# Kernel optimization log

Hardware: AMD Instinct MI355X
Metric: run time of the kernel (lower is better)

The kernel has to match this reference:

```python
import jax, jax.numpy as jnp
import numpy as np

BS, QLEN, DIM, NH = 2, 2048, 1024, 16
HD = DIM // NH


def setup_inputs() -> dict:
    key = jax.random.key(0)
    ks = jax.random.split(key, 6)
    std = 0.02
    return {
        "x": jax.random.normal(ks[0], (BS, QLEN, DIM), dtype=jnp.float32),
        "mask": jnp.ones((BS, QLEN), dtype=jnp.float32),
        "Wq": jax.random.normal(ks[1], (DIM, DIM), dtype=jnp.float32) * std,
        "bq": jnp.zeros((DIM,), dtype=jnp.float32),
        "Wk": jax.random.normal(ks[2], (DIM, DIM), dtype=jnp.float32) * std,
        "bk": jnp.zeros((DIM,), dtype=jnp.float32),
        "Wv": jax.random.normal(ks[3], (DIM, DIM), dtype=jnp.float32) * std,
        "bv": jnp.zeros((DIM,), dtype=jnp.float32),
        "Wo": jax.random.normal(ks[4], (DIM, DIM), dtype=jnp.float32) * std,
        "bo": jnp.zeros((DIM,), dtype=jnp.float32),
    }


def reference(x, mask, Wq, bq, Wk, bk, Wv, bv, Wo, bo):
    bs, qlen, dim = x.shape
    # project and split heads: [bs, nh, len, hd]
    def split_heads(t):
        return t.reshape(bs, -1, NH, HD).transpose(0, 2, 1, 3)

    q = split_heads(x @ Wq + bq) / jnp.sqrt(jnp.float32(HD))
    k = split_heads(x @ Wk + bk)
    v = split_heads(x @ Wv + bv)

    scores = jnp.einsum("bhqd,bhkd->bhqk", q, k)  # [bs, nh, qlen, klen]
    m = mask.reshape(bs, 1, 1, -1)  # 2D mask -> broadcast over heads and q
    scores = scores - 1e30 * (1.0 - m)
    weights = jax.nn.softmax(scores, axis=-1)
    # dropout p=0.0 at inference -> no-op; head_mask is None
    context = jnp.einsum("bhqk,bhkd->bhqd", weights, v)
    context = context.transpose(0, 2, 1, 3).reshape(bs, qlen, NH * HD)
    return context @ Wo + bo
```

## Files before the change

### kernel.cpp

```cpp
#include <hip/hip_runtime.h>
#include <stdint.h>

#define BSZ  2
#define SEQ  2048
#define DIM  1024
#define NHD  16
#define HD   64
#define MTOT (BSZ*SEQ)

using short8  = __attribute__((ext_vector_type(8))) short;
using floatx4 = __attribute__((ext_vector_type(4))) float;

#define QSCALE 0.18033688011112042f
#define BIGM   1.44e30f

__device__ __forceinline__ unsigned short f2bf(float f) {
    unsigned int u = __float_as_uint(f);
    u += 0x7fffu + ((u >> 16) & 1u);
    return (unsigned short)(u >> 16);
}
__device__ __forceinline__ unsigned int pk2r(float a, float b) {
    unsigned int ua = __float_as_uint(a) + 0x8000u;
    unsigned int ub = __float_as_uint(b) + 0x8000u;
    return __builtin_amdgcn_perm(ub, ua, 0x07060302);
}
__device__ __forceinline__ unsigned int cvtpk(float a, float b) {
    unsigned int r;
    asm("v_cvt_pk_bf16_f32 %0, %1, %2" : "=v"(r) : "v"(a), "v"(b));
    return r;
}

__device__ __forceinline__ void gll16(const void* g, const void* lds) {
    unsigned int loff = (unsigned int)(unsigned long long)lds;
    __builtin_amdgcn_global_load_lds(
        (const __attribute__((address_space(1))) unsigned int*)g,
        (__attribute__((address_space(3))) unsigned int*)loff, 16, 0, 0);
}

__global__ __launch_bounds__(256)
void conv_x(const float* __restrict__ X, const float* __restrict__ mask,
            unsigned short* __restrict__ Xbf, float* __restrict__ Pen) {
    size_t i = ((size_t)blockIdx.x * 256 + threadIdx.x) * 8;
    float4 a = *(const float4*)(X + i);
    float4 b = *(const float4*)(X + i + 4);
    uint4 u = {pk2r(a.x, a.y), pk2r(a.z, a.w), pk2r(b.x, b.y), pk2r(b.z, b.w)};
    *(uint4*)(Xbf + i) = u;
    if (blockIdx.x < 2) {
        const size_t j = ((size_t)blockIdx.x * 256 + threadIdx.x) * 8;
        float4 m0 = *(const float4*)(mask + j);
        float4 m1 = *(const float4*)(mask + j + 4);
        float4 r0 = {__builtin_fmaf(m0.x, BIGM, -BIGM), __builtin_fmaf(m0.y, BIGM, -BIGM),
                     __builtin_fmaf(m0.z, BIGM, -BIGM), __builtin_fmaf(m0.w, BIGM, -BIGM)};
        float4 r1 = {__builtin_fmaf(m1.x, BIGM, -BIGM), __builtin_fmaf(m1.y, BIGM, -BIGM),
                     __builtin_fmaf(m1.z, BIGM, -BIGM), __builtin_fmaf(m1.w, BIGM, -BIGM)};
        *(float4*)(Pen + j)     = r0;
        *(float4*)(Pen + j + 4) = r1;
    }
}

__global__ __launch_bounds__(256)
void conv_wt(const float* __restrict__ Wq, const float* __restrict__ Wk,
             const float* __restrict__ Wv, const float* __restrict__ Wo,
             unsigned short* __restrict__ Wt3, unsigned short* __restrict__ Wto)
{
    __shared__ float tile[64 * 65];
    const int z = blockIdx.z;
    const float* W = (z == 0) ? Wq : (z == 1) ? Wk : (z == 2) ? Wv : Wo;
    unsigned short* out = (z < 3) ? (Wt3 + (size_t)z * DIM * DIM) : Wto;
    const int k0 = blockIdx.x * 64, n0 = blockIdx.y * 64;
    const int t = threadIdx.x;
    const int r = t >> 2, c0 = (t & 3) * 16;
#pragma unroll
    for (int j = 0; j < 4; ++j) {
        float4 v = *(const float4*)&W[(size_t)(k0 + r) * DIM + n0 + c0 + j * 4];
        tile[r * 65 + c0 + j * 4 + 0] = v.x;
        tile[r * 65 + c0 + j * 4 + 1] = v.y;
        tile[r * 65 + c0 + j * 4 + 2] = v.z;
        tile[r * 65 + c0 + j * 4 + 3] = v.w;
    }
    __syncthreads();
    unsigned int p[8];
#pragma unroll
    for (int j = 0; j < 8; ++j)
        p[j] = pk2r(tile[(c0 + 2 * j) * 65 + r], tile[(c0 + 2 * j + 1) * 65 + r]);
    uint4 u0 = {p[0], p[1], p[2], p[3]}, u1 = {p[4], p[5], p[6], p[7]};
    unsigned short* dst = out + (size_t)(n0 + r) * DIM + k0 + c0;
    *(uint4*)dst = u0;
    *(uint4*)(dst + 8) = u1;
}

__global__ __launch_bounds__(256)
void qkv_gemm(const unsigned short* __restrict__ Xbf,
              const unsigned short* __restrict__ Wt3,
              const float* __restrict__ bq, const float* __restrict__ bk,
              const float* __restrict__ bv,
              unsigned short* __restrict__ Qb,
              unsigned short* __restrict__ Kb,
              unsigned short* __restrict__ VbT)
{
    __shared__ unsigned short As[2][128 * 32];
    __shared__ unsigned short Bs[2][128 * 32];

    const int t = threadIdx.x, w = t >> 6, lane = t & 63;
    const int lm = lane & 15, grp = lane >> 4;
    const int wm = w >> 1, wn = w & 1;
    const int m0 = blockIdx.x * 128;
    const int mat = blockIdx.y >> 3;
    const int n0 = (blockIdx.y & 7) * 128;
    const unsigned short* Bg = Wt3 + (size_t)mat * DIM * DIM;
    const int lr = lane >> 2, lc = (lane & 3) * 8;
    const int r0 = w * 16;
    const bool swap = (mat != 2);

    const unsigned short* xs0 = Xbf + (size_t)(m0 + r0 + lr) * DIM + lc;
    const unsigned short* xs1 = Xbf + (size_t)(m0 + 64 + r0 + lr) * DIM + lc;
    const unsigned short* ws0 = Bg  + (size_t)(n0 + r0 + lr) * DIM + lc;
    const unsigned short* ws1 = Bg  + (size_t)(n0 + 64 + r0 + lr) * DIM + lc;

    const unsigned short* afb[2];
    const unsigned short* bfb[2];
#pragma unroll
    for (int u = 0; u < 2; ++u) {
        afb[u] = &As[u][(wm * 64 + lm) * 32 + grp * 8];
        bfb[u] = &Bs[u][(wn * 64 + lm) * 32 + grp * 8];
    }

    floatx4 acc[4][4];
#pragma unroll
    for (int i = 0; i < 4; ++i)
#pragma unroll
        for (int j = 0; j < 4; ++j) acc[i][j] = (floatx4){0.f, 0.f, 0.f, 0.f};

#define QKV_STAGE(BUF) do {                                    \
        gll16(xs0, &As[BUF][r0 * 32]);                         \
        gll16(xs1, &As[BUF][(64 + r0) * 32]);                  \
        gll16(ws0, &Bs[BUF][r0 * 32]);                         \
        gll16(ws1, &Bs[BUF][(64 + r0) * 32]);                  \
        xs0 += 32; xs1 += 32; ws0 += 32; ws1 += 32;            \
    } while (0)

#define QKV_BODY(CUR) do {                                                    \
        __syncthreads();                                                      \
        QKV_STAGE(CUR ^ 1);                                                   \
        short8 af[4], bf[4];                                                  \
        _Pragma("unroll")                                                     \
        for (int mt = 0; mt < 4; ++mt)                                        \
            af[mt] = *(const short8*)(afb[CUR] + mt * 512);                   \
        _Pragma("unroll")                                                     \
        for (int nt = 0; nt < 4; ++nt)                                        \
            bf[nt] = *(const short8*)(bfb[CUR] + nt * 512);                   \
        if (swap) {                                                           \
            _Pragma("unroll")                                                 \
            for (int mt = 0; mt < 4; ++mt)                                    \
                _Pragma("unroll")                                             \
                for (int nt = 0; nt < 4; ++nt)                                \
                    acc[mt][nt] = __builtin_amdgcn_mfma_f32_16x16x32_bf16(    \
                        bf[nt], af[mt], acc[mt][nt], 0, 0, 0);                \
        } else {                                                              \
            _Pragma("unroll")                                                 \
            for (int mt = 0; mt < 4; ++mt)                                    \
                _Pragma("unroll")                                             \
                for (int nt = 0; nt < 4; ++nt)                                \
                    acc[mt][nt] = __builtin_amdgcn_mfma_f32_16x16x32_bf16(    \
                        af[mt], bf[nt], acc[mt][nt], 0, 0, 0);                \
        }                                                                     \
    } while (0)

    QKV_STAGE(0);
#pragma unroll 1
    for (int it = 0; it < DIM / 64; ++it) {
        QKV_BODY(0);
        QKV_BODY(1);
    }
#undef QKV_BODY
#undef QKV_STAGE

    if (mat == 2) {
#pragma unroll
        for (int nt = 0; nt < 4; ++nt) {
            const int c = n0 + wn * 64 + nt * 16 + lm;
            const float bb = bv[c];
            const int h = c >> 6, d = c & 63;
#pragma unroll
            for (int mt = 0; mt < 4; ++mt) {
                const int r = m0 + wm * 64 + mt * 16 + grp * 4;
                const int b = r >> 11, s = r & 2047;
                const int si = s & 63, sb = s & ~63;
                const int cg = si >> 4, g = (si >> 2) & 3;
                const int unit = (((cg & 1) << 2) | g) ^ (d & 7);
                const int sph = sb + unit * 8 + ((cg >> 1) << 2);
                uint2 pv;
                pv.x = pk2r(acc[mt][nt][0] + bb, acc[mt][nt][1] + bb);
                pv.y = pk2r(acc[mt][nt][2] + bb, acc[mt][nt][3] + bb);
                *(uint2*)&VbT[(((size_t)(b * NHD + h)) * HD + d) * SEQ + sph] = pv;
            }
        }
    } else {
        const float* bias = (mat == 0) ? bq : bk;
        unsigned short* dst = (mat == 0) ? Qb : Kb;
        const float sc = (mat == 0) ? QSCALE : 1.0f;
#pragma unroll
        for (int nt = 0; nt < 4; ++nt) {
            const int c0 = n0 + wn * 64 + nt * 16 + grp * 4;
            float4 bb = *(const float4*)&bias[c0];
            const int h = c0 >> 6, d0 = c0 & 63;
#pragma unroll
            for (int mt = 0; mt < 4; ++mt) {
                const int r = m0 + wm * 64 + mt * 16 + lm;
                const int b = r >> 11, s = r & 2047;
                uint2 pv;
                pv.x = pk2r((acc[mt][nt][0] + bb.x) * sc, (acc[mt][nt][1] + bb.y) * sc);
                pv.y = pk2r((acc[mt][nt][2] + bb.z) * sc, (acc[mt][nt][3] + bb.w) * sc);
                const int dd = (mat == 0) ? d0
                             : ((((d0 >> 3) ^ (s & 7)) << 3) | (d0 & 7));
                *(uint2*)&dst[(((size_t)(b * NHD + h)) * SEQ + s) * HD + dd] = pv;
            }
        }
    }
}

__global__ __launch_bounds__(256, 4)
void attn(const unsigned short* __restrict__ Qb,
          const unsigned short* __restrict__ Kb,
          const unsigned short* __restrict__ VbT,
          const float* __restrict__ Pen,
          unsigned short* __restrict__ Cb)
{
    __shared__ unsigned short Kt[2][64 * 64];
    __shared__ unsigned short Vt[2][64 * 64];

    const int t = threadIdx.x, w = t >> 6, lane = t & 63;
    const int lm = lane & 15, grp = lane >> 4;
    const int x7 = lm & 7;

    const int lin = blockIdx.y * (int)gridDim.x + blockIdx.x;
    const int swz = (lin & 7) * ((SEQ / 64) * (BSZ * NHD) / 8) + (lin >> 3);
    const int bh = swz >> 5, b = bh >> 4, h = bh & 15;
    const int q0 = (swz & 31) * 64;

    short8 qf[2];
    {
        const unsigned short* qrow = Qb + ((size_t)bh * SEQ + q0 + w * 16 + lm) * HD;
        qf[0] = *(const short8*)(qrow + grp * 8);
        qf[1] = *(const short8*)(qrow + 32 + grp * 8);
    }

    const unsigned int one2 = 0x3f803f80u;
    uint4 onesu = {one2, one2, one2, one2};
    short8 ones = *(const short8*)&onesu;

    floatx4 oacc[4];
#pragma unroll
    for (int i = 0; i < 4; ++i) oacc[i] = (floatx4){0.f, 0.f, 0.f, 0.f};
    floatx4 lacc = (floatx4){0.f, 0.f, 0.f, 0.f};

    const unsigned short* Kg = Kb + (size_t)bh * SEQ * HD;
    const unsigned short* Vg = VbT + (size_t)bh * HD * SEQ;
    const int srow = lane >> 3, scol = (lane & 7) * 8;

    const unsigned short* kp0 = Kg + (size_t)(w * 16 + srow) * HD + scol;
    const unsigned short* kp1 = kp0 + 8 * HD;
    const unsigned short* vp0 = Vg + (size_t)(w * 16 + srow) * SEQ + scol;
    const unsigned short* vp1 = vp0 + 8 * SEQ;

    gll16(kp0, &Kt[0][(w * 16) * 64]);
    gll16(kp1, &Kt[0][(w * 16 + 8) * 64]);
    gll16(vp0, &Vt[0][(w * 16) * 64]);
    gll16(vp1, &Vt[0][(w * 16 + 8) * 64]);
    kp0 += 64 * HD; kp1 += 64 * HD; vp0 += 64; vp1 += 64;

    const unsigned short* kba[2]; const unsigned short* kbb[2];
    const unsigned short* vba[2]; const unsigned short* vbb[2];
#pragma unroll
    for (int u = 0; u < 2; ++u) {
        kba[u] = &Kt[u][lm * 64 + ((grp    ) ^ x7) * 8];
        kbb[u] = &Kt[u][lm * 64 + ((4 + grp) ^ x7) * 8];
        vba[u] = &Vt[u][lm * 64 + ((grp    ) ^ x7) * 8];
        vbb[u] = &Vt[u][lm * 64 + ((4 + grp) ^ x7) * 8];
    }
    const float* mp = Pen + (size_t)b * SEQ + grp * 4;

#define ATTN_BODY(CUR) do {                                                   \
        __syncthreads();                                                      \
        gll16(kp0, &Kt[CUR ^ 1][(w * 16) * 64]);                              \
        gll16(kp1, &Kt[CUR ^ 1][(w * 16 + 8) * 64]);                          \
        gll16(vp0, &Vt[CUR ^ 1][(w * 16) * 64]);                              \
        gll16(vp1, &Vt[CUR ^ 1][(w * 16 + 8) * 64]);                          \
        kp0 += 64 * HD; kp1 += 64 * HD; vp0 += 64; vp1 += 64;                 \
        float4 mdv[4];                                                        \
        _Pragma("unroll")                                                     \
        for (int cg = 0; cg < 4; ++cg)                                        \
            mdv[cg] = *(const float4*)(mp + cg * 16);                         \
        mp += 64;                                                             \
        floatx4 sv[4];                                                        \
        __builtin_amdgcn_s_setprio(1);                                        \
        _Pragma("unroll")                                                     \
        for (int cg = 0; cg < 4; ++cg) {                                      \
            short8 a0 = *(const short8*)(kba[CUR] + cg * 1024);               \
            short8 a1 = *(const short8*)(kbb[CUR] + cg * 1024);               \
            floatx4 s = (floatx4){mdv[cg].x, mdv[cg].y, mdv[cg].z, mdv[cg].w}; \
            s = __builtin_amdgcn_mfma_f32_16x16x32_bf16(a0, qf[0], s, 0, 0, 0); \
            s = __builtin_amdgcn_mfma_f32_16x16x32_bf16(a1, qf[1], s, 0, 0, 0); \
            sv[cg] = s;                                                       \
        }                                                                     \
        __builtin_amdgcn_s_setprio(0);                                        \
        short8 vf[4][2];                                                      \
        _Pragma("unroll")                                                     \
        for (int dg = 0; dg < 4; ++dg) {                                      \
            vf[dg][0] = *(const short8*)(vba[CUR] + dg * 1024);               \
            vf[dg][1] = *(const short8*)(vbb[CUR] + dg * 1024);               \
        }                                                                     \
        float p[4][4];                                                        \
        _Pragma("unroll")                                                     \
        for (int cg = 0; cg < 4; ++cg) {                                      \
            p[cg][0] = __builtin_exp2f(sv[cg][0]);                            \
            p[cg][1] = __builtin_exp2f(sv[cg][1]);                            \
            p[cg][2] = __builtin_exp2f(sv[cg][2]);                            \
            p[cg][3] = __builtin_exp2f(sv[cg][3]);                            \
        }                                                                     \
        uint4 u0, u1;                                                         \
        u0.x = cvtpk(p[0][0], p[0][1]); u0.y = cvtpk(p[0][2], p[0][3]);       \
        u0.z = cvtpk(p[2][0], p[2][1]); u0.w = cvtpk(p[2][2], p[2][3]);       \
        u1.x = cvtpk(p[1][0], p[1][1]); u1.y = cvtpk(p[1][2], p[1][3]);       \
        u1.z = cvtpk(p[3][0], p[3][1]); u1.w = cvtpk(p[3][2], p[3][3]);       \
        short8 ap0 = *(const short8*)&u0;                                     \
        short8 ap1 = *(const short8*)&u1;                                     \
        __builtin_amdgcn_s_setprio(1);                                        \
        _Pragma("unroll")                                                     \
        for (int dg = 0; dg < 4; ++dg) {                                      \
            oacc[dg] = __builtin_amdgcn_mfma_f32_16x16x32_bf16(ap0, vf[dg][0], oacc[dg], 0, 0, 0); \
            oacc[dg] = __builtin_amdgcn_mfma_f32_16x16x32_bf16(ap1, vf[dg][1], oacc[dg], 0, 0, 0); \
        }                                                                     \
        lacc = __builtin_amdgcn_mfma_f32_16x16x32_bf16(ap0, ones, lacc, 0, 0, 0); \
        lacc = __builtin_amdgcn_mfma_f32_16x16x32_bf16(ap1, ones, lacc, 0, 0, 0); \
        __builtin_amdgcn_s_setprio(0);                                        \
    } while (0)

#pragma unroll 1
    for (int it = 0; it < SEQ / 128; ++it) {
        ATTN_BODY(0);
        ATTN_BODY(1);
    }
#undef ATTN_BODY

    float inv[4];
#pragma unroll
    for (int r = 0; r < 4; ++r) inv[r] = (lacc[r] > 0.f) ? 1.0f / lacc[r] : 0.f;
#pragma unroll
    for (int dg = 0; dg < 4; ++dg)
#pragma unroll
        for (int r = 0; r < 4; ++r) {
            const int s = q0 + w * 16 + grp * 4 + r;
            Cb[((size_t)(b * SEQ + s)) * DIM + h * HD + dg * 16 + lm] =
                f2bf(oacc[dg][r] * inv[r]);
        }
}

__global__ __launch_bounds__(256)
void out_gemm(const unsigned short* __restrict__ Cb,
              const unsigned short* __restrict__ Wto,
              const float* __restrict__ bo,
              float* __restrict__ out)
{
    __shared__ unsigned short As[2][128 * 32];
    __shared__ unsigned short Bs[2][64 * 32];

    const int t = threadIdx.x, w = t >> 6, lane = t & 63;
    const int lm = lane & 15, grp = lane >> 4;
    const int m0 = blockIdx.x * 128;
    const int n0 = blockIdx.y * 64;
    const int lr = lane >> 2, lc = (lane & 3) * 8;
    const int r0 = w * 16;

    const unsigned short* cs0 = Cb  + (size_t)(m0 + r0 + lr) * DIM + lc;
    const unsigned short* cs1 = Cb  + (size_t)(m0 + 64 + r0 + lr) * DIM + lc;
    const unsigned short* ws0 = Wto + (size_t)(n0 + r0 + lr) * DIM + lc;

    const unsigned short* afb[2];
    const unsigned short* bfb[2];
#pragma unroll
    for (int u = 0; u < 2; ++u) {
        afb[u] = &As[u][(w * 32 + lm) * 32 + grp * 8];
        bfb[u] = &Bs[u][lm * 32 + grp * 8];
    }

    floatx4 acc[2][4];
#pragma unroll
    for (int i = 0; i < 2; ++i)
#pragma unroll
        for (int j = 0; j < 4; ++j) acc[i][j] = (floatx4){0.f, 0.f, 0.f, 0.f};

#define OUT_STAGE(BUF) do {                                    \
        gll16(cs0, &As[BUF][r0 * 32]);                         \
        gll16(cs1, &As[BUF][(64 + r0) * 32]);                  \
        gll16(ws0, &Bs[BUF][r0 * 32]);                         \
        cs0 += 32; cs1 += 32; ws0 += 32;                       \
    } while (0)

#define OUT_BODY(CUR) do {                                                    \
        __syncthreads();                                                      \
        OUT_STAGE(CUR ^ 1);                                                   \
        short8 af[2], bf[4];                                                  \
        _Pragma("unroll")                                                     \
        for (int mt = 0; mt < 2; ++mt)                                        \
            af[mt] = *(const short8*)(afb[CUR] + mt * 512);                   \
        _Pragma("unroll")                                                     \
        for (int nt = 0; nt < 4; ++nt)                                        \
            bf[nt] = *(const short8*)(bfb[CUR] + nt * 512);                   \
        _Pragma("unroll")                                                     \
        for (int mt = 0; mt < 2; ++mt)                                        \
            _Pragma("unroll")                                                 \
            for (int nt = 0; nt < 4; ++nt)                                    \
                acc[mt][nt] = __builtin_amdgcn_mfma_f32_16x16x32_bf16(        \
                    bf[nt], af[mt], acc[mt][nt], 0, 0, 0);                    \
    } while (0)

    OUT_STAGE(0);
#pragma unroll 1
    for (int it = 0; it < DIM / 64; ++it) {
        OUT_BODY(0);
        OUT_BODY(1);
    }
#undef OUT_BODY
#undef OUT_STAGE

#pragma unroll
    for (int nt = 0; nt < 4; ++nt) {
        const int c0 = n0 + nt * 16 + grp * 4;
        float4 bb = *(const float4*)&bo[c0];
#pragma unroll
        for (int mt = 0; mt < 2; ++mt) {
            const int r = m0 + w * 32 + mt * 16 + lm;
            float4 o = {acc[mt][nt][0] + bb.x, acc[mt][nt][1] + bb.y,
                        acc[mt][nt][2] + bb.z, acc[mt][nt][3] + bb.w};
            *(float4*)&out[(size_t)r * DIM + c0] = o;
        }
    }
}

extern "C" void kernel_launch(void* const* d_in, const int* in_sizes, int n_in,
                              void* d_out, int out_size, void* d_ws, size_t ws_size,
                              hipStream_t stream)
{
    const float* x    = (const float*)d_in[0];
    const float* mask = (const float*)d_in[1];
    const float* Wq   = (const float*)d_in[2];
    const float* bq   = (const float*)d_in[3];
    const float* Wk   = (const float*)d_in[4];
    const float* bk   = (const float*)d_in[5];
    const float* Wv   = (const float*)d_in[6];
    const float* bv   = (const float*)d_in[7];
    const float* Wo   = (const float*)d_in[8];
    const float* bo   = (const float*)d_in[9];
    float* out = (float*)d_out;

    const size_t M1 = (size_t)DIM * DIM;
    unsigned short* Qb  = (unsigned short*)d_ws;
    unsigned short* Kb  = Qb  + 4 * M1;
    unsigned short* VbT = Kb  + 4 * M1;
    unsigned short* Cb  = VbT + 4 * M1;
    unsigned short* Xbf = Cb  + 4 * M1;
    unsigned short* Wt3 = Xbf + 4 * M1;
    unsigned short* Wto = Wt3 + 3 * M1;
    float*          Pen = (float*)(Wto + M1);

    conv_x <<<dim3((MTOT * DIM) / 2048), 256, 0, stream>>>(x, mask, Xbf, Pen);
    conv_wt<<<dim3(16, 16, 4), 256, 0, stream>>>(Wq, Wk, Wv, Wo, Wt3, Wto);
    qkv_gemm<<<dim3(MTOT / 128, 24), 256, 0, stream>>>(Xbf, Wt3, bq, bk, bv, Qb, Kb, VbT);
    attn<<<dim3(SEQ / 64, BSZ * NHD), 256, 0, stream>>>(Qb, Kb, VbT, Pen, Cb);
    out_gemm<<<dim3(MTOT / 128, DIM / 64), 256, 0, stream>>>(Cb, Wto, bo, out);
}
```

Before: 201.7 us.

## Merge conversion kernels into one launch and deepen out_gemm K-step to 64

The separate x/mask conversion and weight-transpose kernels become a single launch that dispatches on block index. This removes one kernel launch and lets the two conversion workloads overlap. Separately, out_gemm now uses four LDS buffers and stages two 32-wide K slices per barrier, which halves the number of __syncthreads calls. The cost is double the LDS use for out_gemm, which may lower occupancy.

New measurement: 203.2 us (median of 2 runs). No clear change (+0.8%).

```diff
diff --git a/kernel.cpp b/kernel.cpp
--- a/kernel.cpp
+++ b/kernel.cpp
@@ -38,37 +38,39 @@
 }
 
 __global__ __launch_bounds__(256)
-void conv_x(const float* __restrict__ X, const float* __restrict__ mask,
-            unsigned short* __restrict__ Xbf, float* __restrict__ Pen) {
-    size_t i = ((size_t)blockIdx.x * 256 + threadIdx.x) * 8;
-    float4 a = *(const float4*)(X + i);
-    float4 b = *(const float4*)(X + i + 4);
-    uint4 u = {pk2r(a.x, a.y), pk2r(a.z, a.w), pk2r(b.x, b.y), pk2r(b.z, b.w)};
-    *(uint4*)(Xbf + i) = u;
-    if (blockIdx.x < 2) {
-        const size_t j = ((size_t)blockIdx.x * 256 + threadIdx.x) * 8;
-        float4 m0 = *(const float4*)(mask + j);
-        float4 m1 = *(const float4*)(mask + j + 4);
-        float4 r0 = {__builtin_fmaf(m0.x, BIGM, -BIGM), __builtin_fmaf(m0.y, BIGM, -BIGM),
-                     __builtin_fmaf(m0.z, BIGM, -BIGM), __builtin_fmaf(m0.w, BIGM, -BIGM)};
-        float4 r1 = {__builtin_fmaf(m1.x, BIGM, -BIGM), __builtin_fmaf(m1.y, BIGM, -BIGM),
-                     __builtin_fmaf(m1.z, BIGM, -BIGM), __builtin_fmaf(m1.w, BIGM, -BIGM)};
-        *(float4*)(Pen + j)     = r0;
-        *(float4*)(Pen + j + 4) = r1;
-    }
-}
-
-__global__ __launch_bounds__(256)
-void conv_wt(const float* __restrict__ Wq, const float* __restrict__ Wk,
-             const float* __restrict__ Wv, const float* __restrict__ Wo,
-             unsigned short* __restrict__ Wt3, unsigned short* __restrict__ Wto)
+void conv_all(const float* __restrict__ X, const float* __restrict__ mask,
+              const float* __restrict__ Wq, const float* __restrict__ Wk,
+              const float* __restrict__ Wv, const float* __restrict__ Wo,
+              unsigned short* __restrict__ Xbf, float* __restrict__ Pen,
+              unsigned short* __restrict__ Wt3, unsigned short* __restrict__ Wto)
 {
     __shared__ float tile[64 * 65];
-    const int z = blockIdx.z;
+    const int t = threadIdx.x;
+    if (blockIdx.x < 2048) {
+        const int bid = blockIdx.x;
+        size_t i = ((size_t)bid * 256 + t) * 8;
+        float4 a = *(const float4*)(X + i);
+        float4 b = *(const float4*)(X + i + 4);
+        uint4 u = {pk2r(a.x, a.y), pk2r(a.z, a.w), pk2r(b.x, b.y), pk2r(b.z, b.w)};
+        *(uint4*)(Xbf + i) = u;
+        if (bid < 2) {
+            const size_t j = ((size_t)bid * 256 + t) * 8;
+            float4 m0 = *(const float4*)(mask + j);
+            float4 m1 = *(const float4*)(mask + j + 4);
+            float4 r0 = {__builtin_fmaf(m0.x, BIGM, -BIGM), __builtin_fmaf(m0.y, BIGM, -BIGM),
+                         __builtin_fmaf(m0.z, BIGM, -BIGM), __builtin_fmaf(m0.w, BIGM, -BIGM)};
+            float4 r1 = {__builtin_fmaf(m1.x, BIGM, -BIGM), __builtin_fmaf(m1.y, BIGM, -BIGM),
+                         __builtin_fmaf(m1.z, BIGM, -BIGM), __builtin_fmaf(m1.w, BIGM, -BIGM)};
+            *(float4*)(Pen + j)     = r0;
+            *(float4*)(Pen + j + 4) = r1;
+        }
+        return;
+    }
+    const int zz = blockIdx.x - 2048;
+    const int z  = zz >> 8;
     const float* W = (z == 0) ? Wq : (z == 1) ? Wk : (z == 2) ? Wv : Wo;
     unsigned short* out = (z < 3) ? (Wt3 + (size_t)z * DIM * DIM) : Wto;
-    const int k0 = blockIdx.x * 64, n0 = blockIdx.y * 64;
-    const int t = threadIdx.x;
+    const int k0 = (zz & 15) * 64, n0 = ((zz >> 4) & 15) * 64;
     const int r = t >> 2, c0 = (t & 3) * 16;
 #pragma unroll
     for (int j = 0; j < 4; ++j) {
@@ -247,7 +249,7 @@
 
     const unsigned int one2 = 0x3f803f80u;
     uint4 onesu = {one2, one2, one2, one2};
-    short8 ones = *(const short8*)&onesu;
+    const short8 ones = *(const short8*)&onesu;
 
     floatx4 oacc[4];
 #pragma unroll
@@ -362,8 +364,8 @@
               const float* __restrict__ bo,
               float* __restrict__ out)
 {
-    __shared__ unsigned short As[2][128 * 32];
-    __shared__ unsigned short Bs[2][64 * 32];
+    __shared__ unsigned short As[4][128 * 32];
+    __shared__ unsigned short Bs[4][64 * 32];
 
     const int t = threadIdx.x, w = t >> 6, lane = t & 63;
     const int lm = lane & 15, grp = lane >> 4;
@@ -376,10 +378,10 @@
     const unsigned short* cs1 = Cb  + (size_t)(m0 + 64 + r0 + lr) * DIM + lc;
     const unsigned short* ws0 = Wto + (size_t)(n0 + r0 + lr) * DIM + lc;
 
-    const unsigned short* afb[2];
-    const unsigned short* bfb[2];
-#pragma unroll
-    for (int u = 0; u < 2; ++u) {
+    const unsigned short* afb[4];
+    const unsigned short* bfb[4];
+#pragma unroll
+    for (int u = 0; u < 4; ++u) {
         afb[u] = &As[u][(w * 32 + lm) * 32 + grp * 8];
         bfb[u] = &Bs[u][lm * 32 + grp * 8];
     }
@@ -397,16 +399,14 @@
         cs0 += 32; cs1 += 32; ws0 += 32;                       \
     } while (0)
 
-#define OUT_BODY(CUR) do {                                                    \
-        __syncthreads();                                                      \
-        OUT_STAGE(CUR ^ 1);                                                   \
+#define OUT_HALF(BUF) do {                                                    \
         short8 af[2], bf[4];                                                  \
         _Pragma("unroll")                                                     \
         for (int mt = 0; mt < 2; ++mt)                                        \
-            af[mt] = *(const short8*)(afb[CUR] + mt * 512);                   \
+            af[mt] = *(const short8*)(afb[BUF] + mt * 512);                   \
         _Pragma("unroll")                                                     \
         for (int nt = 0; nt < 4; ++nt)                                        \
-            bf[nt] = *(const short8*)(bfb[CUR] + nt * 512);                   \
+            bf[nt] = *(const short8*)(bfb[BUF] + nt * 512);                   \
         _Pragma("unroll")                                                     \
         for (int mt = 0; mt < 2; ++mt)                                        \
             _Pragma("unroll")                                                 \
@@ -415,13 +415,23 @@
                     bf[nt], af[mt], acc[mt][nt], 0, 0, 0);                    \
     } while (0)
 
+#define OUT_BODY(B0, B1, W0, W1) do {                                         \
+        __syncthreads();                                                      \
+        OUT_STAGE(W0);                                                        \
+        OUT_STAGE(W1);                                                        \
+        OUT_HALF(B0);                                                         \
+        OUT_HALF(B1);                                                         \
+    } while (0)
+
     OUT_STAGE(0);
+    OUT_STAGE(1);
 #pragma unroll 1
-    for (int it = 0; it < DIM / 64; ++it) {
-        OUT_BODY(0);
-        OUT_BODY(1);
+    for (int it = 0; it < DIM / 128; ++it) {
+        OUT_BODY(0, 1, 2, 3);
+        OUT_BODY(2, 3, 0, 1);
     }
 #undef OUT_BODY
+#undef OUT_HALF
 #undef OUT_STAGE
 
 #pragma unroll
@@ -464,8 +474,8 @@
     unsigned short* Wto = Wt3 + 3 * M1;
     float*          Pen = (float*)(Wto + M1);
 
-    conv_x <<<dim3((MTOT * DIM) / 2048), 256, 0, stream>>>(x, mask, Xbf, Pen);
-    conv_wt<<<dim3(16, 16, 4), 256, 0, stream>>>(Wq, Wk, Wv, Wo, Wt3, Wto);
+    conv_all<<<dim3(3072), 256, 0, stream>>>(x, mask, Wq, Wk, Wv, Wo,
+                                             Xbf, Pen, Wt3, Wto);
     qkv_gemm<<<dim3(MTOT / 128, 24), 256, 0, stream>>>(Xbf, Wt3, bq, bk, bv, Qb, Kb, VbT);
     attn<<<dim3(SEQ / 64, BSZ * NHD), 256, 0, stream>>>(Qb, Kb, VbT, Pen, Cb);
     out_gemm<<<dim3(MTOT / 128, DIM / 64), 256, 0, stream>>>(Cb, Wto, bo, out);
```
